# Performance work log

Hardware: AMD Instinct MI355X
Metric: run time of the kernel (lower is better)

The kernel has to match this reference:

```python
import jax, jax.numpy as jnp
import numpy as np

# The original module wraps a CvxpyLayer solving, per batch element:
#   min_y  c^T y - sum(entr(y) + entr(1-y))   (use_entropy=True)
#   s.t.   a' y + b' >= 0,  lb <= y <= ub
# where the wrapper passes a' = -a, b' = -b, i.e. the constraints are a y + b <= 0,
# with lb=0, ub=1. With binary entropy regularization the KKT stationarity gives
# the closed form y*(lam) = sigmoid(-(c + a^T lam)) for dual vars lam >= 0, and the
# dual is maximized by projected gradient ascent (grad = a y* + b). This is the
# standard smooth/batched-GPU-friendly formulation of the same convex program.

NUM_ITERS = 100  # fixed dual ascent iterations (jit-friendly)
STEP = 0.05      # dual step size


def _solve(a, b, c):
    # a: [B, M, N], b: [B, M], c: [B, N]
    def body(lam, _):
        # y*(lam) = sigmoid(-(c + a^T lam))   [B, N]
        y = jax.nn.sigmoid(-(c + jnp.einsum('bmn,bm->bn', a, lam)))
        # dual gradient: a y + b               [B, M]
        g = jnp.einsum('bmn,bn->bm', a, y) + b
        lam = jnp.maximum(lam + STEP * g, 0.0)
        return lam, None

    lam0 = jnp.zeros_like(b)
    lam, _ = jax.lax.scan(body, lam0, None, length=NUM_ITERS)
    y = jax.nn.sigmoid(-(c + jnp.einsum('bmn,bm->bn', a, lam)))
    return y


def setup_inputs() -> dict:
    key = jax.random.key(0)
    ka, kb, kc = jax.random.split(key, 3)
    B, M, N = 2048, 128, 256
    a = jax.random.normal(ka, (B, M, N), dtype=jnp.float32)
    b = jax.random.normal(kb, (B, M), dtype=jnp.float32)
    c = jax.random.normal(kc, (B, N), dtype=jnp.float32)
    return {"a": a, "b": b, "c": c}


def reference(a, b, c):
    y = _solve(a, b, c).astype(jnp.float32)
    status = jnp.zeros((a.shape[0],), dtype=jnp.int32)
    return (y, status)
```

## Files before the change

kernel.cpp:

```cpp
#include <hip/hip_runtime.h>


#define BB 2048
#define MM 128
#define NN 256

__global__ __launch_bounds__(512, 2) void cvx_dual_ascent(
    const float* __restrict__ A,
    const float* __restrict__ Bv,
    const float* __restrict__ C,
    float* __restrict__ out)
{
    const int bi  = blockIdx.x;
    const int tid = threadIdx.x;
    const int w   = tid >> 6;
    const int l   = tid & 63;
    const int c   = tid >> 1;
    const int myrow = (l >> 1) & 15;

    __shared__ float zp_s[8][260];
    __shared__ float y_s[NN];
    __shared__ float lam_s[8][16];
    __shared__ float scr_s[512];

    const float* Ab = A + (size_t)bi * (MM * NN);
    unsigned long long a0  = (unsigned long long)(Ab + (16*w + 0)  * NN + 4*l);
    unsigned long long a4  = (unsigned long long)(Ab + (16*w + 4)  * NN + 4*l);
    unsigned long long a8  = (unsigned long long)(Ab + (16*w + 8)  * NN + 4*l);
    unsigned long long a12 = (unsigned long long)(Ab + (16*w + 12) * NN + 4*l);
    unsigned lamrd = (unsigned)(size_t)&lam_s[w][0];
    unsigned zpw   = (unsigned)(size_t)&zp_s[w][4*l];
    unsigned zprd  = (unsigned)(size_t)&zp_s[(tid & 1) * 4][c];
    unsigned ysw   = (unsigned)(size_t)&y_s[c];
    unsigned ysr   = (unsigned)(size_t)&y_s[4*l];
    unsigned lamw  = (unsigned)(size_t)&lam_s[w][myrow];
    unsigned scw   = (unsigned)(size_t)&scr_s[tid];
    unsigned scrd  = (unsigned)(size_t)&scr_s[tid ^ 32];
    unsigned long long outa = (unsigned long long)(out + (size_t)bi * NN + c);
    float cr  = C[bi * NN + c];
    float sbv = 0.05f * Bv[bi * MM + 16*w + myrow];
    float lam = 0.f;
    int   cnt = 100;

    if (tid < 128) lam_s[tid >> 4][tid & 15] = 0.f;
    __syncthreads();

    asm volatile(
        "global_load_dwordx4 v[36:39], %[a0], off\n\t"
        "global_load_dwordx4 v[40:43], %[a0], off offset:1024\n\t"
        "global_load_dwordx4 v[44:47], %[a0], off offset:2048\n\t"
        "global_load_dwordx4 v[48:51], %[a0], off offset:3072\n\t"
        "global_load_dwordx4 v[52:55], %[a4], off\n\t"
        "global_load_dwordx4 v[56:59], %[a4], off offset:1024\n\t"
        "global_load_dwordx4 v[60:63], %[a4], off offset:2048\n\t"
        "global_load_dwordx4 v[64:67], %[a4], off offset:3072\n\t"
        "global_load_dwordx4 v[68:71], %[a8], off\n\t"
        "global_load_dwordx4 v[72:75], %[a8], off offset:1024\n\t"
        "global_load_dwordx4 v[76:79], %[a8], off offset:2048\n\t"
        "global_load_dwordx4 v[80:83], %[a8], off offset:3072\n\t"
        "global_load_dwordx4 v[84:87], %[a12], off\n\t"
        "global_load_dwordx4 v[88:91], %[a12], off offset:1024\n\t"
        "global_load_dwordx4 v[92:95], %[a12], off offset:2048\n\t"
        "global_load_dwordx4 v[96:99], %[a12], off offset:3072\n\t"
        "s_waitcnt vmcnt(0)\n\t"
        ".LTOP%=:\n\t"
        "ds_read_b128 v[100:103], %[lamrd]\n\t"
        "ds_read_b128 v[104:107], %[lamrd] offset:16\n\t"
        "ds_read_b128 v[108:111], %[lamrd] offset:32\n\t"
        "ds_read_b128 v[112:115], %[lamrd] offset:48\n\t"
        "s_waitcnt lgkmcnt(0)\n\t"
        "v_mul_f32 v116, v36, v100\n\t"
        "v_mul_f32 v117, v37, v100\n\t"
        "v_mul_f32 v118, v38, v100\n\t"
        "v_mul_f32 v119, v39, v100\n\t"
        "v_fmac_f32 v116, v40, v101\n\t"
        "v_fmac_f32 v117, v41, v101\n\t"
        "v_fmac_f32 v118, v42, v101\n\t"
        "v_fmac_f32 v119, v43, v101\n\t"
        "v_fmac_f32 v116, v44, v102\n\t"
        "v_fmac_f32 v117, v45, v102\n\t"
        "v_fmac_f32 v118, v46, v102\n\t"
        "v_fmac_f32 v119, v47, v102\n\t"
        "v_fmac_f32 v116, v48, v103\n\t"
        "v_fmac_f32 v117, v49, v103\n\t"
        "v_fmac_f32 v118, v50, v103\n\t"
        "v_fmac_f32 v119, v51, v103\n\t"
        "v_fmac_f32 v116, v52, v104\n\t"
        "v_fmac_f32 v117, v53, v104\n\t"
        "v_fmac_f32 v118, v54, v104\n\t"
        "v_fmac_f32 v119, v55, v104\n\t"
        "v_fmac_f32 v116, v56, v105\n\t"
        "v_fmac_f32 v117, v57, v105\n\t"
        "v_fmac_f32 v118, v58, v105\n\t"
        "v_fmac_f32 v119, v59, v105\n\t"
        "v_fmac_f32 v116, v60, v106\n\t"
        "v_fmac_f32 v117, v61, v106\n\t"
        "v_fmac_f32 v118, v62, v106\n\t"
        "v_fmac_f32 v119, v63, v106\n\t"
        "v_fmac_f32 v116, v64, v107\n\t"
        "v_fmac_f32 v117, v65, v107\n\t"
        "v_fmac_f32 v118, v66, v107\n\t"
        "v_fmac_f32 v119, v67, v107\n\t"
        "v_fmac_f32 v116, v68, v108\n\t"
        "v_fmac_f32 v117, v69, v108\n\t"
        "v_fmac_f32 v118, v70, v108\n\t"
        "v_fmac_f32 v119, v71, v108\n\t"
        "v_fmac_f32 v116, v72, v109\n\t"
        "v_fmac_f32 v117, v73, v109\n\t"
        "v_fmac_f32 v118, v74, v109\n\t"
        "v_fmac_f32 v119, v75, v109\n\t"
        "v_fmac_f32 v116, v76, v110\n\t"
        "v_fmac_f32 v117, v77, v110\n\t"
        "v_fmac_f32 v118, v78, v110\n\t"
        "v_fmac_f32 v119, v79, v110\n\t"
        "v_fmac_f32 v116, v80, v111\n\t"
        "v_fmac_f32 v117, v81, v111\n\t"
        "v_fmac_f32 v118, v82, v111\n\t"
        "v_fmac_f32 v119, v83, v111\n\t"
        "v_fmac_f32 v116, v84, v112\n\t"
        "v_fmac_f32 v117, v85, v112\n\t"
        "v_fmac_f32 v118, v86, v112\n\t"
        "v_fmac_f32 v119, v87, v112\n\t"
        "v_fmac_f32 v116, v88, v113\n\t"
        "v_fmac_f32 v117, v89, v113\n\t"
        "v_fmac_f32 v118, v90, v113\n\t"
        "v_fmac_f32 v119, v91, v113\n\t"
        "v_fmac_f32 v116, v92, v114\n\t"
        "v_fmac_f32 v117, v93, v114\n\t"
        "v_fmac_f32 v118, v94, v114\n\t"
        "v_fmac_f32 v119, v95, v114\n\t"
        "v_fmac_f32 v116, v96, v115\n\t"
        "v_fmac_f32 v117, v97, v115\n\t"
        "v_fmac_f32 v118, v98, v115\n\t"
        "v_fmac_f32 v119, v99, v115\n\t"
        "ds_write_b128 %[zpw], v[116:119]\n\t"
        "s_waitcnt lgkmcnt(0)\n\t"
        "s_barrier\n\t"
        "ds_read_b32 v120, %[zprd]\n\t"
        "ds_read_b32 v121, %[zprd] offset:1040\n\t"
        "ds_read_b32 v122, %[zprd] offset:2080\n\t"
        "ds_read_b32 v123, %[zprd] offset:3120\n\t"
        "s_waitcnt lgkmcnt(0)\n\t"
        "v_add_f32 v120, v120, v121\n\t"
        "v_add_f32 v122, v122, v123\n\t"
        "v_add_f32 v120, v120, v122\n\t"
        "ds_swizzle_b32 v121, v120 offset:0x041F\n\t"
        "s_waitcnt lgkmcnt(0)\n\t"
        "v_add_f32 v120, v120, v121\n\t"
        "v_add_f32 v121, %[cr], v120\n\t"
        "v_mul_f32 v121, %[l2e], v121\n\t"
        "v_exp_f32 v121, v121\n\t"
        "s_nop 1\n\t"
        "v_add_f32 v121, 1.0, v121\n\t"
        "v_rcp_f32 v121, v121\n\t"
        "s_nop 1\n\t"
        "s_cmp_eq_u32 %[cnt], 0\n\t"
        "s_cbranch_scc1 .LEXIT%=\n\t"
        "ds_write_b32 %[ysw], v121\n\t"
        "s_waitcnt lgkmcnt(0)\n\t"
        "s_barrier\n\t"
        "ds_read_b128 v[116:119], %[ysr]\n\t"
        "s_waitcnt lgkmcnt(0)\n\t"
        "v_mul_f32 v100, v36, v116\n\t"
        "v_mul_f32 v101, v40, v116\n\t"
        "v_mul_f32 v102, v44, v116\n\t"
        "v_mul_f32 v103, v48, v116\n\t"
        "v_mul_f32 v104, v52, v116\n\t"
        "v_mul_f32 v105, v56, v116\n\t"
        "v_mul_f32 v106, v60, v116\n\t"
        "v_mul_f32 v107, v64, v116\n\t"
        "v_mul_f32 v108, v68, v116\n\t"
        "v_mul_f32 v109, v72, v116\n\t"
        "v_mul_f32 v110, v76, v116\n\t"
        "v_mul_f32 v111, v80, v116\n\t"
        "v_mul_f32 v112, v84, v116\n\t"
        "v_mul_f32 v113, v88, v116\n\t"
        "v_mul_f32 v114, v92, v116\n\t"
        "v_mul_f32 v115, v96, v116\n\t"
        "v_fmac_f32 v100, v37, v117\n\t"
        "v_fmac_f32 v101, v41, v117\n\t"
        "v_fmac_f32 v102, v45, v117\n\t"
        "v_fmac_f32 v103, v49, v117\n\t"
        "v_fmac_f32 v104, v53, v117\n\t"
        "v_fmac_f32 v105, v57, v117\n\t"
        "v_fmac_f32 v106, v61, v117\n\t"
        "v_fmac_f32 v107, v65, v117\n\t"
        "v_fmac_f32 v108, v69, v117\n\t"
        "v_fmac_f32 v109, v73, v117\n\t"
        "v_fmac_f32 v110, v77, v117\n\t"
        "v_fmac_f32 v111, v81, v117\n\t"
        "v_fmac_f32 v112, v85, v117\n\t"
        "v_fmac_f32 v113, v89, v117\n\t"
        "v_fmac_f32 v114, v93, v117\n\t"
        "v_fmac_f32 v115, v97, v117\n\t"
        "v_fmac_f32 v100, v38, v118\n\t"
        "v_fmac_f32 v101, v42, v118\n\t"
        "v_fmac_f32 v102, v46, v118\n\t"
        "v_fmac_f32 v103, v50, v118\n\t"
        "v_fmac_f32 v104, v54, v118\n\t"
        "v_fmac_f32 v105, v58, v118\n\t"
        "v_fmac_f32 v106, v62, v118\n\t"
        "v_fmac_f32 v107, v66, v118\n\t"
        "v_fmac_f32 v108, v70, v118\n\t"
        "v_fmac_f32 v109, v74, v118\n\t"
        "v_fmac_f32 v110, v78, v118\n\t"
        "v_fmac_f32 v111, v82, v118\n\t"
        "v_fmac_f32 v112, v86, v118\n\t"
        "v_fmac_f32 v113, v90, v118\n\t"
        "v_fmac_f32 v114, v94, v118\n\t"
        "v_fmac_f32 v115, v98, v118\n\t"
        "v_fmac_f32 v100, v39, v119\n\t"
        "v_fmac_f32 v101, v43, v119\n\t"
        "v_fmac_f32 v102, v47, v119\n\t"
        "v_fmac_f32 v103, v51, v119\n\t"
        "v_fmac_f32 v104, v55, v119\n\t"
        "v_fmac_f32 v105, v59, v119\n\t"
        "v_fmac_f32 v106, v63, v119\n\t"
        "v_fmac_f32 v107, v67, v119\n\t"
        "v_fmac_f32 v108, v71, v119\n\t"
        "v_fmac_f32 v109, v75, v119\n\t"
        "v_fmac_f32 v110, v79, v119\n\t"
        "v_fmac_f32 v111, v83, v119\n\t"
        "v_fmac_f32 v112, v87, v119\n\t"
        "v_fmac_f32 v113, v91, v119\n\t"
        "v_fmac_f32 v114, v95, v119\n\t"
        "v_fmac_f32 v115, v99, v119\n\t"
        "v_cndmask_b32 v120, v100, v108, %[mb4]\n\t"
        "v_cndmask_b32 v121, v101, v109, %[mb4]\n\t"
        "v_cndmask_b32 v122, v102, v110, %[mb4]\n\t"
        "v_cndmask_b32 v123, v103, v111, %[mb4]\n\t"
        "v_cndmask_b32 v124, v108, v100, %[mb4]\n\t"
        "v_cndmask_b32 v125, v109, v101, %[mb4]\n\t"
        "v_cndmask_b32 v126, v110, v102, %[mb4]\n\t"
        "v_cndmask_b32 v127, v111, v103, %[mb4]\n\t"
        "ds_swizzle_b32 v124, v124 offset:0x401F\n\t"
        "ds_swizzle_b32 v125, v125 offset:0x401F\n\t"
        "ds_swizzle_b32 v126, v126 offset:0x401F\n\t"
        "ds_swizzle_b32 v127, v127 offset:0x401F\n\t"
        "v_cndmask_b32 v116, v104, v112, %[mb4]\n\t"
        "v_cndmask_b32 v117, v105, v113, %[mb4]\n\t"
        "v_cndmask_b32 v118, v106, v114, %[mb4]\n\t"
        "v_cndmask_b32 v119, v107, v115, %[mb4]\n\t"
        "v_cndmask_b32 v108, v112, v104, %[mb4]\n\t"
        "v_cndmask_b32 v109, v113, v105, %[mb4]\n\t"
        "v_cndmask_b32 v110, v114, v106, %[mb4]\n\t"
        "v_cndmask_b32 v111, v115, v107, %[mb4]\n\t"
        "ds_swizzle_b32 v108, v108 offset:0x401F\n\t"
        "ds_swizzle_b32 v109, v109 offset:0x401F\n\t"
        "ds_swizzle_b32 v110, v110 offset:0x401F\n\t"
        "ds_swizzle_b32 v111, v111 offset:0x401F\n\t"
        "s_waitcnt lgkmcnt(0)\n\t"
        "v_add_f32 v100, v120, v124\n\t"
        "v_add_f32 v101, v121, v125\n\t"
        "v_add_f32 v102, v122, v126\n\t"
        "v_add_f32 v103, v123, v127\n\t"
        "v_add_f32 v104, v116, v108\n\t"
        "v_add_f32 v105, v117, v109\n\t"
        "v_add_f32 v106, v118, v110\n\t"
        "v_add_f32 v107, v119, v111\n\t"
        "v_cndmask_b32 v120, v100, v104, %[mb3]\n\t"
        "v_cndmask_b32 v121, v101, v105, %[mb3]\n\t"
        "v_cndmask_b32 v122, v102, v106, %[mb3]\n\t"
        "v_cndmask_b32 v123, v103, v107, %[mb3]\n\t"
        "v_cndmask_b32 v124, v104, v100, %[mb3]\n\t"
        "v_cndmask_b32 v125, v105, v101, %[mb3]\n\t"
        "v_cndmask_b32 v126, v106, v102, %[mb3]\n\t"
        "v_cndmask_b32 v127, v107, v103, %[mb3]\n\t"
        "ds_swizzle_b32 v124, v124 offset:0x201F\n\t"
        "ds_swizzle_b32 v125, v125 offset:0x201F\n\t"
        "ds_swizzle_b32 v126, v126 offset:0x201F\n\t"
        "ds_swizzle_b32 v127, v127 offset:0x201F\n\t"
        "s_waitcnt lgkmcnt(0)\n\t"
        "v_add_f32 v100, v120, v124\n\t"
        "v_add_f32 v101, v121, v125\n\t"
        "v_add_f32 v102, v122, v126\n\t"
        "v_add_f32 v103, v123, v127\n\t"
        "v_cndmask_b32 v120, v100, v102, %[mb2]\n\t"
        "v_cndmask_b32 v121, v101, v103, %[mb2]\n\t"
        "v_cndmask_b32 v122, v102, v100, %[mb2]\n\t"
        "v_cndmask_b32 v123, v103, v101, %[mb2]\n\t"
        "ds_swizzle_b32 v122, v122 offset:0x101F\n\t"
        "ds_swizzle_b32 v123, v123 offset:0x101F\n\t"
        "s_waitcnt lgkmcnt(0)\n\t"
        "v_add_f32 v100, v120, v122\n\t"
        "v_add_f32 v101, v121, v123\n\t"
        "v_cndmask_b32 v120, v100, v101, %[mb1]\n\t"
        "v_cndmask_b32 v121, v101, v100, %[mb1]\n\t"
        "ds_swizzle_b32 v121, v121 offset:0x081F\n\t"
        "s_waitcnt lgkmcnt(0)\n\t"
        "v_add_f32 v100, v120, v121\n\t"
        "ds_swizzle_b32 v101, v100 offset:0x041F\n\t"
        "s_waitcnt lgkmcnt(0)\n\t"
        "v_add_f32 v100, v100, v101\n\t"
        "ds_write_b32 %[scw], v100\n\t"
        "s_waitcnt lgkmcnt(0)\n\t"
        "ds_read_b32 v101, %[scrd]\n\t"
        "s_waitcnt lgkmcnt(0)\n\t"
        "v_add_f32 v100, v100, v101\n\t"
        "v_fmac_f32 %[lam], %[step], v100\n\t"
        "v_add_f32 %[lam], %[sb], %[lam]\n\t"
        "v_max_f32 %[lam], 0, %[lam]\n\t"
        "ds_write_b32 %[lamw], %[lam]\n\t"
        "s_waitcnt lgkmcnt(0)\n\t"
        "s_sub_u32 %[cnt], %[cnt], 1\n\t"
        "s_branch .LTOP%=\n\t"
        ".LEXIT%=:\n\t"
        "global_store_dword %[outa], v121, off\n\t"
        "s_waitcnt vmcnt(0)\n\t"
        : [lam] "+v"(lam), [cnt] "+s"(cnt)
        : [a0] "v"(a0), [a4] "v"(a4), [a8] "v"(a8), [a12] "v"(a12),
          [lamrd] "v"(lamrd), [zpw] "v"(zpw), [zprd] "v"(zprd),
          [ysw] "v"(ysw), [ysr] "v"(ysr), [lamw] "v"(lamw),
          [scw] "v"(scw), [scrd] "v"(scrd), [outa] "v"(outa),
          [cr] "v"(cr), [sb] "v"(sbv),
          [step] "s"(0.05f), [l2e] "s"(1.4426950408889634f),
          [mb4] "s"(0xFFFF0000FFFF0000ull), [mb3] "s"(0xFF00FF00FF00FF00ull),
          [mb2] "s"(0xF0F0F0F0F0F0F0F0ull), [mb1] "s"(0xCCCCCCCCCCCCCCCCull)
        : "memory", "scc",
          "v36","v37","v38","v39","v40","v41","v42","v43","v44","v45",
          "v46","v47","v48","v49","v50","v51","v52","v53","v54","v55",
          "v56","v57","v58","v59","v60","v61","v62","v63","v64","v65",
          "v66","v67","v68","v69","v70","v71","v72","v73","v74","v75",
          "v76","v77","v78","v79","v80","v81","v82","v83","v84","v85",
          "v86","v87","v88","v89","v90","v91","v92","v93","v94","v95",
          "v96","v97","v98","v99","v100","v101","v102","v103","v104",
          "v105","v106","v107","v108","v109","v110","v111","v112","v113",
          "v114","v115","v116","v117","v118","v119","v120","v121","v122",
          "v123","v124","v125","v126","v127");

    if (tid == 0) out[(size_t)BB * NN + bi] = 0.0f;
}

extern "C" void kernel_launch(void* const* d_in, const int* in_sizes, int n_in,
                              void* d_out, int out_size, void* d_ws, size_t ws_size,
                              hipStream_t stream) {
    const float* A  = (const float*)d_in[0];
    const float* Bv = (const float*)d_in[1];
    const float* C  = (const float*)d_in[2];
    float* out = (float*)d_out;

    cvx_dual_ascent<<<dim3(BB), dim3(512), 0, stream>>>(A, Bv, C, out);
}
```

Measured before the change: 511.0 us.

## Keep dual variables in SGPRs and replace LDS swizzle reductions with DPP/permlane

The per-iteration lambda broadcast through LDS (ds_write, ds_read_b128 ×4) is replaced by v_readlane into 16 SGPRs, which are then used directly as scalar operands in the A^T·lam FMAs. The butterfly reduction for the A·y gradient is rebuilt around v_permlane32_swap and v_permlane16_swap, with DPP row_ror and quad_perm replacing most ds_swizzle ops and the LDS scratch exchange. The lane-to-row mapping changes so each row's result lands in lanes spaced four apart. This removes LDS round-trips and lgkmcnt waits from the serial 100-iteration loop, at the cost of readlane latency, extra s_nop hazard padding and 16 clobbered SGPRs.

```diff
diff --git a/kernel.cpp b/kernel.cpp
--- a/kernel.cpp
+++ b/kernel.cpp
@@ -16,33 +16,26 @@
     const int w   = tid >> 6;
     const int l   = tid & 63;
     const int c   = tid >> 1;
-    const int myrow = (l >> 1) & 15;
+    const int myrow = (l >> 2) & 15;
 
     __shared__ float zp_s[8][260];
     __shared__ float y_s[NN];
-    __shared__ float lam_s[8][16];
-    __shared__ float scr_s[512];
 
     const float* Ab = A + (size_t)bi * (MM * NN);
     unsigned long long a0  = (unsigned long long)(Ab + (16*w + 0)  * NN + 4*l);
     unsigned long long a4  = (unsigned long long)(Ab + (16*w + 4)  * NN + 4*l);
     unsigned long long a8  = (unsigned long long)(Ab + (16*w + 8)  * NN + 4*l);
     unsigned long long a12 = (unsigned long long)(Ab + (16*w + 12) * NN + 4*l);
-    unsigned lamrd = (unsigned)(size_t)&lam_s[w][0];
     unsigned zpw   = (unsigned)(size_t)&zp_s[w][4*l];
     unsigned zprd  = (unsigned)(size_t)&zp_s[(tid & 1) * 4][c];
     unsigned ysw   = (unsigned)(size_t)&y_s[c];
     unsigned ysr   = (unsigned)(size_t)&y_s[4*l];
-    unsigned lamw  = (unsigned)(size_t)&lam_s[w][myrow];
-    unsigned scw   = (unsigned)(size_t)&scr_s[tid];
-    unsigned scrd  = (unsigned)(size_t)&scr_s[tid ^ 32];
     unsigned long long outa = (unsigned long long)(out + (size_t)bi * NN + c);
     float cr  = C[bi * NN + c];
     float sbv = 0.05f * Bv[bi * MM + 16*w + myrow];
     float lam = 0.f;
     int   cnt = 100;
 
-    if (tid < 128) lam_s[tid >> 4][tid & 15] = 0.f;
     __syncthreads();
 
     asm volatile(
@@ -62,77 +55,80 @@
         "global_load_dwordx4 v[88:91], %[a12], off offset:1024\n\t"
         "global_load_dwordx4 v[92:95], %[a12], off offset:2048\n\t"
         "global_load_dwordx4 v[96:99], %[a12], off offset:3072\n\t"
+        "s_mov_b32 s80, 0\n\t"  "s_mov_b32 s81, 0\n\t"
+        "s_mov_b32 s82, 0\n\t"  "s_mov_b32 s83, 0\n\t"
+        "s_mov_b32 s84, 0\n\t"  "s_mov_b32 s85, 0\n\t"
+        "s_mov_b32 s86, 0\n\t"  "s_mov_b32 s87, 0\n\t"
+        "s_mov_b32 s88, 0\n\t"  "s_mov_b32 s89, 0\n\t"
+        "s_mov_b32 s90, 0\n\t"  "s_mov_b32 s91, 0\n\t"
+        "s_mov_b32 s92, 0\n\t"  "s_mov_b32 s93, 0\n\t"
+        "s_mov_b32 s94, 0\n\t"  "s_mov_b32 s95, 0\n\t"
         "s_waitcnt vmcnt(0)\n\t"
         ".LTOP%=:\n\t"
-        "ds_read_b128 v[100:103], %[lamrd]\n\t"
-        "ds_read_b128 v[104:107], %[lamrd] offset:16\n\t"
-        "ds_read_b128 v[108:111], %[lamrd] offset:32\n\t"
-        "ds_read_b128 v[112:115], %[lamrd] offset:48\n\t"
-        "s_waitcnt lgkmcnt(0)\n\t"
-        "v_mul_f32 v116, v36, v100\n\t"
-        "v_mul_f32 v117, v37, v100\n\t"
-        "v_mul_f32 v118, v38, v100\n\t"
-        "v_mul_f32 v119, v39, v100\n\t"
-        "v_fmac_f32 v116, v40, v101\n\t"
-        "v_fmac_f32 v117, v41, v101\n\t"
-        "v_fmac_f32 v118, v42, v101\n\t"
-        "v_fmac_f32 v119, v43, v101\n\t"
-        "v_fmac_f32 v116, v44, v102\n\t"
-        "v_fmac_f32 v117, v45, v102\n\t"
-        "v_fmac_f32 v118, v46, v102\n\t"
-        "v_fmac_f32 v119, v47, v102\n\t"
-        "v_fmac_f32 v116, v48, v103\n\t"
-        "v_fmac_f32 v117, v49, v103\n\t"
-        "v_fmac_f32 v118, v50, v103\n\t"
-        "v_fmac_f32 v119, v51, v103\n\t"
-        "v_fmac_f32 v116, v52, v104\n\t"
-        "v_fmac_f32 v117, v53, v104\n\t"
-        "v_fmac_f32 v118, v54, v104\n\t"
-        "v_fmac_f32 v119, v55, v104\n\t"
-        "v_fmac_f32 v116, v56, v105\n\t"
-        "v_fmac_f32 v117, v57, v105\n\t"
-        "v_fmac_f32 v118, v58, v105\n\t"
-        "v_fmac_f32 v119, v59, v105\n\t"
-        "v_fmac_f32 v116, v60, v106\n\t"
-        "v_fmac_f32 v117, v61, v106\n\t"
-        "v_fmac_f32 v118, v62, v106\n\t"
-        "v_fmac_f32 v119, v63, v106\n\t"
-        "v_fmac_f32 v116, v64, v107\n\t"
-        "v_fmac_f32 v117, v65, v107\n\t"
-        "v_fmac_f32 v118, v66, v107\n\t"
-        "v_fmac_f32 v119, v67, v107\n\t"
-        "v_fmac_f32 v116, v68, v108\n\t"
-        "v_fmac_f32 v117, v69, v108\n\t"
-        "v_fmac_f32 v118, v70, v108\n\t"
-        "v_fmac_f32 v119, v71, v108\n\t"
-        "v_fmac_f32 v116, v72, v109\n\t"
-        "v_fmac_f32 v117, v73, v109\n\t"
-        "v_fmac_f32 v118, v74, v109\n\t"
-        "v_fmac_f32 v119, v75, v109\n\t"
-        "v_fmac_f32 v116, v76, v110\n\t"
-        "v_fmac_f32 v117, v77, v110\n\t"
-        "v_fmac_f32 v118, v78, v110\n\t"
-        "v_fmac_f32 v119, v79, v110\n\t"
-        "v_fmac_f32 v116, v80, v111\n\t"
-        "v_fmac_f32 v117, v81, v111\n\t"
-        "v_fmac_f32 v118, v82, v111\n\t"
-        "v_fmac_f32 v119, v83, v111\n\t"
-        "v_fmac_f32 v116, v84, v112\n\t"
-        "v_fmac_f32 v117, v85, v112\n\t"
-        "v_fmac_f32 v118, v86, v112\n\t"
-        "v_fmac_f32 v119, v87, v112\n\t"
-        "v_fmac_f32 v116, v88, v113\n\t"
-        "v_fmac_f32 v117, v89, v113\n\t"
-        "v_fmac_f32 v118, v90, v113\n\t"
-        "v_fmac_f32 v119, v91, v113\n\t"
-        "v_fmac_f32 v116, v92, v114\n\t"
-        "v_fmac_f32 v117, v93, v114\n\t"
-        "v_fmac_f32 v118, v94, v114\n\t"
-        "v_fmac_f32 v119, v95, v114\n\t"
-        "v_fmac_f32 v116, v96, v115\n\t"
-        "v_fmac_f32 v117, v97, v115\n\t"
-        "v_fmac_f32 v118, v98, v115\n\t"
-        "v_fmac_f32 v119, v99, v115\n\t"
+        "v_mul_f32 v116, s80, v36\n\t"
+        "v_mul_f32 v117, s80, v37\n\t"
+        "v_mul_f32 v118, s80, v38\n\t"
+        "v_mul_f32 v119, s80, v39\n\t"
+        "v_fmac_f32 v116, s81, v40\n\t"
+        "v_fmac_f32 v117, s81, v41\n\t"
+        "v_fmac_f32 v118, s81, v42\n\t"
+        "v_fmac_f32 v119, s81, v43\n\t"
+        "v_fmac_f32 v116, s82, v44\n\t"
+        "v_fmac_f32 v117, s82, v45\n\t"
+        "v_fmac_f32 v118, s82, v46\n\t"
+        "v_fmac_f32 v119, s82, v47\n\t"
+        "v_fmac_f32 v116, s83, v48\n\t"
+        "v_fmac_f32 v117, s83, v49\n\t"
+        "v_fmac_f32 v118, s83, v50\n\t"
+        "v_fmac_f32 v119, s83, v51\n\t"
+        "v_fmac_f32 v116, s84, v52\n\t"
+        "v_fmac_f32 v117, s84, v53\n\t"
+        "v_fmac_f32 v118, s84, v54\n\t"
+        "v_fmac_f32 v119, s84, v55\n\t"
+        "v_fmac_f32 v116, s85, v56\n\t"
+        "v_fmac_f32 v117, s85, v57\n\t"
+        "v_fmac_f32 v118, s85, v58\n\t"
+        "v_fmac_f32 v119, s85, v59\n\t"
+        "v_fmac_f32 v116, s86, v60\n\t"
+        "v_fmac_f32 v117, s86, v61\n\t"
+        "v_fmac_f32 v118, s86, v62\n\t"
+        "v_fmac_f32 v119, s86, v63\n\t"
+        "v_fmac_f32 v116, s87, v64\n\t"
+        "v_fmac_f32 v117, s87, v65\n\t"
+        "v_fmac_f32 v118, s87, v66\n\t"
+        "v_fmac_f32 v119, s87, v67\n\t"
+        "v_fmac_f32 v116, s88, v68\n\t"
+        "v_fmac_f32 v117, s88, v69\n\t"
+        "v_fmac_f32 v118, s88, v70\n\t"
+        "v_fmac_f32 v119, s88, v71\n\t"
+        "v_fmac_f32 v116, s89, v72\n\t"
+        "v_fmac_f32 v117, s89, v73\n\t"
+        "v_fmac_f32 v118, s89, v74\n\t"
+        "v_fmac_f32 v119, s89, v75\n\t"
+        "v_fmac_f32 v116, s90, v76\n\t"
+        "v_fmac_f32 v117, s90, v77\n\t"
+        "v_fmac_f32 v118, s90, v78\n\t"
+        "v_fmac_f32 v119, s90, v79\n\t"
+        "v_fmac_f32 v116, s91, v80\n\t"
+        "v_fmac_f32 v117, s91, v81\n\t"
+        "v_fmac_f32 v118, s91, v82\n\t"
+        "v_fmac_f32 v119, s91, v83\n\t"
+        "v_fmac_f32 v116, s92, v84\n\t"
+        "v_fmac_f32 v117, s92, v85\n\t"
+        "v_fmac_f32 v118, s92, v86\n\t"
+        "v_fmac_f32 v119, s92, v87\n\t"
+        "v_fmac_f32 v116, s93, v88\n\t"
+        "v_fmac_f32 v117, s93, v89\n\t"
+        "v_fmac_f32 v118, s93, v90\n\t"
+        "v_fmac_f32 v119, s93, v91\n\t"
+        "v_fmac_f32 v116, s94, v92\n\t"
+        "v_fmac_f32 v117, s94, v93\n\t"
+        "v_fmac_f32 v118, s94, v94\n\t"
+        "v_fmac_f32 v119, s94, v95\n\t"
+        "v_fmac_f32 v116, s95, v96\n\t"
+        "v_fmac_f32 v117, s95, v97\n\t"
+        "v_fmac_f32 v118, s95, v98\n\t"
+        "v_fmac_f32 v119, s95, v99\n\t"
         "ds_write_b128 %[zpw], v[116:119]\n\t"
         "s_waitcnt lgkmcnt(0)\n\t"
         "s_barrier\n\t"
@@ -144,8 +140,8 @@
         "v_add_f32 v120, v120, v121\n\t"
         "v_add_f32 v122, v122, v123\n\t"
         "v_add_f32 v120, v120, v122\n\t"
-        "ds_swizzle_b32 v121, v120 offset:0x041F\n\t"
-        "s_waitcnt lgkmcnt(0)\n\t"
+        "s_nop 1\n\t"
+        "v_mov_b32_dpp v121, v120 quad_perm:[1,0,3,2] row_mask:0xf bank_mask:0xf\n\t"
         "v_add_f32 v120, v120, v121\n\t"
         "v_add_f32 v121, %[cr], v120\n\t"
         "v_mul_f32 v121, %[l2e], v121\n\t"
@@ -225,83 +221,71 @@
         "v_fmac_f32 v113, v91, v119\n\t"
         "v_fmac_f32 v114, v95, v119\n\t"
         "v_fmac_f32 v115, v99, v119\n\t"
-        "v_cndmask_b32 v120, v100, v108, %[mb4]\n\t"
-        "v_cndmask_b32 v121, v101, v109, %[mb4]\n\t"
-        "v_cndmask_b32 v122, v102, v110, %[mb4]\n\t"
-        "v_cndmask_b32 v123, v103, v111, %[mb4]\n\t"
-        "v_cndmask_b32 v124, v108, v100, %[mb4]\n\t"
-        "v_cndmask_b32 v125, v109, v101, %[mb4]\n\t"
-        "v_cndmask_b32 v126, v110, v102, %[mb4]\n\t"
-        "v_cndmask_b32 v127, v111, v103, %[mb4]\n\t"
-        "ds_swizzle_b32 v124, v124 offset:0x401F\n\t"
-        "ds_swizzle_b32 v125, v125 offset:0x401F\n\t"
-        "ds_swizzle_b32 v126, v126 offset:0x401F\n\t"
-        "ds_swizzle_b32 v127, v127 offset:0x401F\n\t"
-        "v_cndmask_b32 v116, v104, v112, %[mb4]\n\t"
-        "v_cndmask_b32 v117, v105, v113, %[mb4]\n\t"
-        "v_cndmask_b32 v118, v106, v114, %[mb4]\n\t"
-        "v_cndmask_b32 v119, v107, v115, %[mb4]\n\t"
-        "v_cndmask_b32 v108, v112, v104, %[mb4]\n\t"
-        "v_cndmask_b32 v109, v113, v105, %[mb4]\n\t"
-        "v_cndmask_b32 v110, v114, v106, %[mb4]\n\t"
-        "v_cndmask_b32 v111, v115, v107, %[mb4]\n\t"
-        "ds_swizzle_b32 v108, v108 offset:0x401F\n\t"
-        "ds_swizzle_b32 v109, v109 offset:0x401F\n\t"
-        "ds_swizzle_b32 v110, v110 offset:0x401F\n\t"
-        "ds_swizzle_b32 v111, v111 offset:0x401F\n\t"
-        "s_waitcnt lgkmcnt(0)\n\t"
+        "s_nop 1\n\t"
+        "v_permlane32_swap_b32 v100, v108\n\t"
+        "v_permlane32_swap_b32 v101, v109\n\t"
+        "v_permlane32_swap_b32 v102, v110\n\t"
+        "v_permlane32_swap_b32 v103, v111\n\t"
+        "v_permlane32_swap_b32 v104, v112\n\t"
+        "v_permlane32_swap_b32 v105, v113\n\t"
+        "v_permlane32_swap_b32 v106, v114\n\t"
+        "v_permlane32_swap_b32 v107, v115\n\t"
+        "v_add_f32 v100, v100, v108\n\t"
+        "v_add_f32 v101, v101, v109\n\t"
+        "v_add_f32 v102, v102, v110\n\t"
+        "v_add_f32 v103, v103, v111\n\t"
+        "v_add_f32 v104, v104, v112\n\t"
+        "v_add_f32 v105, v105, v113\n\t"
+        "v_add_f32 v106, v106, v114\n\t"
+        "v_add_f32 v107, v107, v115\n\t"
+        "v_permlane16_swap_b32 v100, v104\n\t"
+        "v_permlane16_swap_b32 v101, v105\n\t"
+        "v_permlane16_swap_b32 v102, v106\n\t"
+        "v_permlane16_swap_b32 v103, v107\n\t"
+        "v_add_f32 v100, v100, v104\n\t"
+        "v_add_f32 v101, v101, v105\n\t"
+        "v_add_f32 v102, v102, v106\n\t"
+        "v_add_f32 v103, v103, v107\n\t"
+        "v_cndmask_b32 v120, v100, v102, %[mb3]\n\t"
+        "v_cndmask_b32 v121, v102, v100, %[mb3]\n\t"
+        "v_cndmask_b32 v122, v101, v103, %[mb3]\n\t"
+        "v_cndmask_b32 v123, v103, v101, %[mb3]\n\t"
+        "s_nop 1\n\t"
+        "v_mov_b32_dpp v124, v121 row_ror:8 row_mask:0xf bank_mask:0xf\n\t"
+        "v_mov_b32_dpp v125, v123 row_ror:8 row_mask:0xf bank_mask:0xf\n\t"
         "v_add_f32 v100, v120, v124\n\t"
-        "v_add_f32 v101, v121, v125\n\t"
-        "v_add_f32 v102, v122, v126\n\t"
-        "v_add_f32 v103, v123, v127\n\t"
-        "v_add_f32 v104, v116, v108\n\t"
-        "v_add_f32 v105, v117, v109\n\t"
-        "v_add_f32 v106, v118, v110\n\t"
-        "v_add_f32 v107, v119, v111\n\t"
-        "v_cndmask_b32 v120, v100, v104, %[mb3]\n\t"
-        "v_cndmask_b32 v121, v101, v105, %[mb3]\n\t"
-        "v_cndmask_b32 v122, v102, v106, %[mb3]\n\t"
-        "v_cndmask_b32 v123, v103, v107, %[mb3]\n\t"
-        "v_cndmask_b32 v124, v104, v100, %[mb3]\n\t"
-        "v_cndmask_b32 v125, v105, v101, %[mb3]\n\t"
-        "v_cndmask_b32 v126, v106, v102, %[mb3]\n\t"
-        "v_cndmask_b32 v127, v107, v103, %[mb3]\n\t"
-        "ds_swizzle_b32 v124, v124 offset:0x201F\n\t"
-        "ds_swizzle_b32 v125, v125 offset:0x201F\n\t"
-        "ds_swizzle_b32 v126, v126 offset:0x201F\n\t"
-        "ds_swizzle_b32 v127, v127 offset:0x201F\n\t"
-        "s_waitcnt lgkmcnt(0)\n\t"
-        "v_add_f32 v100, v120, v124\n\t"
-        "v_add_f32 v101, v121, v125\n\t"
-        "v_add_f32 v102, v122, v126\n\t"
-        "v_add_f32 v103, v123, v127\n\t"
-        "v_cndmask_b32 v120, v100, v102, %[mb2]\n\t"
-        "v_cndmask_b32 v121, v101, v103, %[mb2]\n\t"
-        "v_cndmask_b32 v122, v102, v100, %[mb2]\n\t"
-        "v_cndmask_b32 v123, v103, v101, %[mb2]\n\t"
-        "ds_swizzle_b32 v122, v122 offset:0x101F\n\t"
-        "ds_swizzle_b32 v123, v123 offset:0x101F\n\t"
-        "s_waitcnt lgkmcnt(0)\n\t"
-        "v_add_f32 v100, v120, v122\n\t"
-        "v_add_f32 v101, v121, v123\n\t"
-        "v_cndmask_b32 v120, v100, v101, %[mb1]\n\t"
-        "v_cndmask_b32 v121, v101, v100, %[mb1]\n\t"
-        "ds_swizzle_b32 v121, v121 offset:0x081F\n\t"
+        "v_add_f32 v101, v122, v125\n\t"
+        "v_cndmask_b32 v120, v100, v101, %[mb2]\n\t"
+        "v_cndmask_b32 v121, v101, v100, %[mb2]\n\t"
+        "ds_swizzle_b32 v121, v121 offset:0x101F\n\t"
         "s_waitcnt lgkmcnt(0)\n\t"
         "v_add_f32 v100, v120, v121\n\t"
-        "ds_swizzle_b32 v101, v100 offset:0x041F\n\t"
-        "s_waitcnt lgkmcnt(0)\n\t"
-        "v_add_f32 v100, v100, v101\n\t"
-        "ds_write_b32 %[scw], v100\n\t"
-        "s_waitcnt lgkmcnt(0)\n\t"
-        "ds_read_b32 v101, %[scrd]\n\t"
-        "s_waitcnt lgkmcnt(0)\n\t"
-        "v_add_f32 v100, v100, v101\n\t"
+        "s_nop 1\n\t"
+        "v_mov_b32_dpp v121, v100 quad_perm:[2,3,0,1] row_mask:0xf bank_mask:0xf\n\t"
+        "v_add_f32 v100, v100, v121\n\t"
+        "s_nop 1\n\t"
+        "v_mov_b32_dpp v121, v100 quad_perm:[1,0,3,2] row_mask:0xf bank_mask:0xf\n\t"
+        "v_add_f32 v100, v100, v121\n\t"
         "v_fmac_f32 %[lam], %[step], v100\n\t"
         "v_add_f32 %[lam], %[sb], %[lam]\n\t"
         "v_max_f32 %[lam], 0, %[lam]\n\t"
-        "ds_write_b32 %[lamw], %[lam]\n\t"
-        "s_waitcnt lgkmcnt(0)\n\t"
+        "s_nop 1\n\t"
+        "v_readlane_b32 s80, %[lam], 0\n\t"
+        "v_readlane_b32 s81, %[lam], 4\n\t"
+        "v_readlane_b32 s82, %[lam], 8\n\t"
+        "v_readlane_b32 s83, %[lam], 12\n\t"
+        "v_readlane_b32 s84, %[lam], 16\n\t"
+        "v_readlane_b32 s85, %[lam], 20\n\t"
+        "v_readlane_b32 s86, %[lam], 24\n\t"
+        "v_readlane_b32 s87, %[lam], 28\n\t"
+        "v_readlane_b32 s88, %[lam], 32\n\t"
+        "v_readlane_b32 s89, %[lam], 36\n\t"
+        "v_readlane_b32 s90, %[lam], 40\n\t"
+        "v_readlane_b32 s91, %[lam], 44\n\t"
+        "v_readlane_b32 s92, %[lam], 48\n\t"
+        "v_readlane_b32 s93, %[lam], 52\n\t"
+        "v_readlane_b32 s94, %[lam], 56\n\t"
+        "v_readlane_b32 s95, %[lam], 60\n\t"
         "s_sub_u32 %[cnt], %[cnt], 1\n\t"
         "s_branch .LTOP%=\n\t"
         ".LEXIT%=:\n\t"
@@ -309,14 +293,14 @@
         "s_waitcnt vmcnt(0)\n\t"
         : [lam] "+v"(lam), [cnt] "+s"(cnt)
         : [a0] "v"(a0), [a4] "v"(a4), [a8] "v"(a8), [a12] "v"(a12),
-          [lamrd] "v"(lamrd), [zpw] "v"(zpw), [zprd] "v"(zprd),
-          [ysw] "v"(ysw), [ysr] "v"(ysr), [lamw] "v"(lamw),
-          [scw] "v"(scw), [scrd] "v"(scrd), [outa] "v"(outa),
+          [zpw] "v"(zpw), [zprd] "v"(zprd),
+          [ysw] "v"(ysw), [ysr] "v"(ysr), [outa] "v"(outa),
           [cr] "v"(cr), [sb] "v"(sbv),
           [step] "s"(0.05f), [l2e] "s"(1.4426950408889634f),
-          [mb4] "s"(0xFFFF0000FFFF0000ull), [mb3] "s"(0xFF00FF00FF00FF00ull),
-          [mb2] "s"(0xF0F0F0F0F0F0F0F0ull), [mb1] "s"(0xCCCCCCCCCCCCCCCCull)
+          [mb3] "s"(0xFF00FF00FF00FF00ull), [mb2] "s"(0xF0F0F0F0F0F0F0F0ull)
         : "memory", "scc",
+          "s80","s81","s82","s83","s84","s85","s86","s87",
+          "s88","s89","s90","s91","s92","s93","s94","s95",
           "v36","v37","v38","v39","v40","v41","v42","v43","v44","v45",
           "v46","v47","v48","v49","v50","v51","v52","v53","v54","v55",
           "v56","v57","v58","v59","v60","v61","v62","v63","v64","v65",
```

Measured after the change: 539.7 us. 1.06x slower.

## Compute sigmoid redundantly per wave to drop second barrier; double-buffer partials; permlane reductions

Applied to the files above, without the earlier changes.

Each wave now reads all eight waves' partial z-sums directly (double-buffered shared array toggled by xor) and computes the full 256-element sigmoid vector locally, eliminating the y_s write/barrier/read round trip per iteration. The cross-lane row reduction is rebuilt using permlane32/permlane16 swaps and DPP moves instead of chains of ds_swizzle and LDS scratch exchange. This trades one barrier and several LDS round trips per iteration for redundant exp/rcp work across waves and more LDS read bandwidth; only wave 0 stores the output.

```diff
diff --git a/kernel.cpp b/kernel.cpp
--- a/kernel.cpp
+++ b/kernel.cpp
@@ -15,13 +15,10 @@
     const int tid = threadIdx.x;
     const int w   = tid >> 6;
     const int l   = tid & 63;
-    const int c   = tid >> 1;
-    const int myrow = (l >> 1) & 15;
-
-    __shared__ float zp_s[8][260];
-    __shared__ float y_s[NN];
+    const int myrow = (l >> 2) & 15;
+
+    __shared__ float zp2_s[2][8][256];
     __shared__ float lam_s[8][16];
-    __shared__ float scr_s[512];
 
     const float* Ab = A + (size_t)bi * (MM * NN);
     unsigned long long a0  = (unsigned long long)(Ab + (16*w + 0)  * NN + 4*l);
@@ -29,23 +26,24 @@
     unsigned long long a8  = (unsigned long long)(Ab + (16*w + 8)  * NN + 4*l);
     unsigned long long a12 = (unsigned long long)(Ab + (16*w + 12) * NN + 4*l);
     unsigned lamrd = (unsigned)(size_t)&lam_s[w][0];
-    unsigned zpw   = (unsigned)(size_t)&zp_s[w][4*l];
-    unsigned zprd  = (unsigned)(size_t)&zp_s[(tid & 1) * 4][c];
-    unsigned ysw   = (unsigned)(size_t)&y_s[c];
-    unsigned ysr   = (unsigned)(size_t)&y_s[4*l];
+    unsigned zpw   = (unsigned)(size_t)&zp2_s[0][w][4*l];
+    unsigned zprd  = (unsigned)(size_t)&zp2_s[0][0][4*l];
     unsigned lamw  = (unsigned)(size_t)&lam_s[w][myrow];
-    unsigned scw   = (unsigned)(size_t)&scr_s[tid];
-    unsigned scrd  = (unsigned)(size_t)&scr_s[tid ^ 32];
-    unsigned long long outa = (unsigned long long)(out + (size_t)bi * NN + c);
-    float cr  = C[bi * NN + c];
+    unsigned long long outa = (unsigned long long)(out + (size_t)bi * NN + 4*l);
+    const float4 c4 = *reinterpret_cast<const float4*>(&C[bi * NN + 4*l]);
+    float c0 = c4.x, c1 = c4.y, c2 = c4.z, c3 = c4.w;
     float sbv = 0.05f * Bv[bi * MM + 16*w + myrow];
     float lam = 0.f;
+    float wvf = (float)0;
+    int   wvv = w;
     int   cnt = 100;
+    (void)wvf;
 
     if (tid < 128) lam_s[tid >> 4][tid & 15] = 0.f;
     __syncthreads();
 
     asm volatile(
+        "v_readfirstlane_b32 s78, %[wvv]\n\t"
         "global_load_dwordx4 v[36:39], %[a0], off\n\t"
         "global_load_dwordx4 v[40:43], %[a0], off offset:1024\n\t"
         "global_load_dwordx4 v[44:47], %[a0], off offset:2048\n\t"
@@ -136,31 +134,70 @@
         "ds_write_b128 %[zpw], v[116:119]\n\t"
         "s_waitcnt lgkmcnt(0)\n\t"
         "s_barrier\n\t"
-        "ds_read_b32 v120, %[zprd]\n\t"
-        "ds_read_b32 v121, %[zprd] offset:1040\n\t"
-        "ds_read_b32 v122, %[zprd] offset:2080\n\t"
-        "ds_read_b32 v123, %[zprd] offset:3120\n\t"
-        "s_waitcnt lgkmcnt(0)\n\t"
-        "v_add_f32 v120, v120, v121\n\t"
-        "v_add_f32 v122, v122, v123\n\t"
-        "v_add_f32 v120, v120, v122\n\t"
-        "ds_swizzle_b32 v121, v120 offset:0x041F\n\t"
-        "s_waitcnt lgkmcnt(0)\n\t"
-        "v_add_f32 v120, v120, v121\n\t"
-        "v_add_f32 v121, %[cr], v120\n\t"
-        "v_mul_f32 v121, %[l2e], v121\n\t"
-        "v_exp_f32 v121, v121\n\t"
-        "s_nop 1\n\t"
-        "v_add_f32 v121, 1.0, v121\n\t"
-        "v_rcp_f32 v121, v121\n\t"
+        "ds_read_b128 v[100:103], %[zprd]\n\t"
+        "ds_read_b128 v[104:107], %[zprd] offset:1024\n\t"
+        "ds_read_b128 v[108:111], %[zprd] offset:2048\n\t"
+        "ds_read_b128 v[112:115], %[zprd] offset:3072\n\t"
+        "ds_read_b128 v[120:123], %[zprd] offset:4096\n\t"
+        "ds_read_b128 v[124:127], %[zprd] offset:5120\n\t"
+        "s_waitcnt lgkmcnt(0)\n\t"
+        "v_add_f32 v100, v100, v104\n\t"
+        "v_add_f32 v101, v101, v105\n\t"
+        "v_add_f32 v102, v102, v106\n\t"
+        "v_add_f32 v103, v103, v107\n\t"
+        "v_add_f32 v108, v108, v112\n\t"
+        "v_add_f32 v109, v109, v113\n\t"
+        "v_add_f32 v110, v110, v114\n\t"
+        "v_add_f32 v111, v111, v115\n\t"
+        "v_add_f32 v120, v120, v124\n\t"
+        "v_add_f32 v121, v121, v125\n\t"
+        "v_add_f32 v122, v122, v126\n\t"
+        "v_add_f32 v123, v123, v127\n\t"
+        "v_add_f32 v100, v100, v108\n\t"
+        "v_add_f32 v101, v101, v109\n\t"
+        "v_add_f32 v102, v102, v110\n\t"
+        "v_add_f32 v103, v103, v111\n\t"
+        "ds_read_b128 v[104:107], %[zprd] offset:6144\n\t"
+        "ds_read_b128 v[108:111], %[zprd] offset:7168\n\t"
+        "v_add_f32 v100, v100, v120\n\t"
+        "v_add_f32 v101, v101, v121\n\t"
+        "v_add_f32 v102, v102, v122\n\t"
+        "v_add_f32 v103, v103, v123\n\t"
+        "s_waitcnt lgkmcnt(0)\n\t"
+        "v_add_f32 v104, v104, v108\n\t"
+        "v_add_f32 v105, v105, v109\n\t"
+        "v_add_f32 v106, v106, v110\n\t"
+        "v_add_f32 v107, v107, v111\n\t"
+        "v_add_f32 v100, v100, v104\n\t"
+        "v_add_f32 v101, v101, v105\n\t"
+        "v_add_f32 v102, v102, v106\n\t"
+        "v_add_f32 v103, v103, v107\n\t"
+        "v_xor_b32 %[zpw], 0x2000, %[zpw]\n\t"
+        "v_xor_b32 %[zprd], 0x2000, %[zprd]\n\t"
+        "v_add_f32 v116, %[c0], v100\n\t"
+        "v_add_f32 v117, %[c1], v101\n\t"
+        "v_add_f32 v118, %[c2], v102\n\t"
+        "v_add_f32 v119, %[c3], v103\n\t"
+        "v_mul_f32 v116, %[l2e], v116\n\t"
+        "v_mul_f32 v117, %[l2e], v117\n\t"
+        "v_mul_f32 v118, %[l2e], v118\n\t"
+        "v_mul_f32 v119, %[l2e], v119\n\t"
+        "v_exp_f32 v116, v116\n\t"
+        "v_exp_f32 v117, v117\n\t"
+        "v_exp_f32 v118, v118\n\t"
+        "v_exp_f32 v119, v119\n\t"
+        "s_nop 1\n\t"
+        "v_add_f32 v116, 1.0, v116\n\t"
+        "v_add_f32 v117, 1.0, v117\n\t"
+        "v_add_f32 v118, 1.0, v118\n\t"
+        "v_add_f32 v119, 1.0, v119\n\t"
+        "v_rcp_f32 v116, v116\n\t"
+        "v_rcp_f32 v117, v117\n\t"
+        "v_rcp_f32 v118, v118\n\t"
+        "v_rcp_f32 v119, v119\n\t"
         "s_nop 1\n\t"
         "s_cmp_eq_u32 %[cnt], 0\n\t"
         "s_cbranch_scc1 .LEXIT%=\n\t"
-        "ds_write_b32 %[ysw], v121\n\t"
-        "s_waitcnt lgkmcnt(0)\n\t"
-        "s_barrier\n\t"
-        "ds_read_b128 v[116:119], %[ysr]\n\t"
-        "s_waitcnt lgkmcnt(0)\n\t"
         "v_mul_f32 v100, v36, v116\n\t"
         "v_mul_f32 v101, v40, v116\n\t"
         "v_mul_f32 v102, v44, v116\n\t"
@@ -225,98 +262,71 @@
         "v_fmac_f32 v113, v91, v119\n\t"
         "v_fmac_f32 v114, v95, v119\n\t"
         "v_fmac_f32 v115, v99, v119\n\t"
-        "v_cndmask_b32 v120, v100, v108, %[mb4]\n\t"
-        "v_cndmask_b32 v121, v101, v109, %[mb4]\n\t"
-        "v_cndmask_b32 v122, v102, v110, %[mb4]\n\t"
-        "v_cndmask_b32 v123, v103, v111, %[mb4]\n\t"
-        "v_cndmask_b32 v124, v108, v100, %[mb4]\n\t"
-        "v_cndmask_b32 v125, v109, v101, %[mb4]\n\t"
-        "v_cndmask_b32 v126, v110, v102, %[mb4]\n\t"
-        "v_cndmask_b32 v127, v111, v103, %[mb4]\n\t"
-        "ds_swizzle_b32 v124, v124 offset:0x401F\n\t"
-        "ds_swizzle_b32 v125, v125 offset:0x401F\n\t"
-        "ds_swizzle_b32 v126, v126 offset:0x401F\n\t"
-        "ds_swizzle_b32 v127, v127 offset:0x401F\n\t"
-        "v_cndmask_b32 v116, v104, v112, %[mb4]\n\t"
-        "v_cndmask_b32 v117, v105, v113, %[mb4]\n\t"
-        "v_cndmask_b32 v118, v106, v114, %[mb4]\n\t"
-        "v_cndmask_b32 v119, v107, v115, %[mb4]\n\t"
-        "v_cndmask_b32 v108, v112, v104, %[mb4]\n\t"
-        "v_cndmask_b32 v109, v113, v105, %[mb4]\n\t"
-        "v_cndmask_b32 v110, v114, v106, %[mb4]\n\t"
-        "v_cndmask_b32 v111, v115, v107, %[mb4]\n\t"
-        "ds_swizzle_b32 v108, v108 offset:0x401F\n\t"
-        "ds_swizzle_b32 v109, v109 offset:0x401F\n\t"
-        "ds_swizzle_b32 v110, v110 offset:0x401F\n\t"
-        "ds_swizzle_b32 v111, v111 offset:0x401F\n\t"
-        "s_waitcnt lgkmcnt(0)\n\t"
+        "s_nop 1\n\t"
+        "v_permlane32_swap_b32 v100, v108\n\t"
+        "v_permlane32_swap_b32 v101, v109\n\t"
+        "v_permlane32_swap_b32 v102, v110\n\t"
+        "v_permlane32_swap_b32 v103, v111\n\t"
+        "v_permlane32_swap_b32 v104, v112\n\t"
+        "v_permlane32_swap_b32 v105, v113\n\t"
+        "v_permlane32_swap_b32 v106, v114\n\t"
+        "v_permlane32_swap_b32 v107, v115\n\t"
+        "v_add_f32 v100, v100, v108\n\t"
+        "v_add_f32 v101, v101, v109\n\t"
+        "v_add_f32 v102, v102, v110\n\t"
+        "v_add_f32 v103, v103, v111\n\t"
+        "v_add_f32 v104, v104, v112\n\t"
+        "v_add_f32 v105, v105, v113\n\t"
+        "v_add_f32 v106, v106, v114\n\t"
+        "v_add_f32 v107, v107, v115\n\t"
+        "v_permlane16_swap_b32 v100, v104\n\t"
+        "v_permlane16_swap_b32 v101, v105\n\t"
+        "v_permlane16_swap_b32 v102, v106\n\t"
+        "v_permlane16_swap_b32 v103, v107\n\t"
+        "v_add_f32 v100, v100, v104\n\t"
+        "v_add_f32 v101, v101, v105\n\t"
+        "v_add_f32 v102, v102, v106\n\t"
+        "v_add_f32 v103, v103, v107\n\t"
+        "v_cndmask_b32 v120, v100, v102, %[mb3]\n\t"
+        "v_cndmask_b32 v121, v102, v100, %[mb3]\n\t"
+        "v_cndmask_b32 v122, v101, v103, %[mb3]\n\t"
+        "v_cndmask_b32 v123, v103, v101, %[mb3]\n\t"
+        "s_nop 1\n\t"
+        "v_mov_b32_dpp v124, v121 row_ror:8 row_mask:0xf bank_mask:0xf\n\t"
+        "v_mov_b32_dpp v125, v123 row_ror:8 row_mask:0xf bank_mask:0xf\n\t"
         "v_add_f32 v100, v120, v124\n\t"
-        "v_add_f32 v101, v121, v125\n\t"
-        "v_add_f32 v102, v122, v126\n\t"
-        "v_add_f32 v103, v123, v127\n\t"
-        "v_add_f32 v104, v116, v108\n\t"
-        "v_add_f32 v105, v117, v109\n\t"
-        "v_add_f32 v106, v118, v110\n\t"
-        "v_add_f32 v107, v119, v111\n\t"
-        "v_cndmask_b32 v120, v100, v104, %[mb3]\n\t"
-        "v_cndmask_b32 v121, v101, v105, %[mb3]\n\t"
-        "v_cndmask_b32 v122, v102, v106, %[mb3]\n\t"
-        "v_cndmask_b32 v123, v103, v107, %[mb3]\n\t"
-        "v_cndmask_b32 v124, v104, v100, %[mb3]\n\t"
-        "v_cndmask_b32 v125, v105, v101, %[mb3]\n\t"
-        "v_cndmask_b32 v126, v106, v102, %[mb3]\n\t"
-        "v_cndmask_b32 v127, v107, v103, %[mb3]\n\t"
-        "ds_swizzle_b32 v124, v124 offset:0x201F\n\t"
-        "ds_swizzle_b32 v125, v125 offset:0x201F\n\t"
-        "ds_swizzle_b32 v126, v126 offset:0x201F\n\t"
-        "ds_swizzle_b32 v127, v127 offset:0x201F\n\t"
-        "s_waitcnt lgkmcnt(0)\n\t"
-        "v_add_f32 v100, v120, v124\n\t"
-        "v_add_f32 v101, v121, v125\n\t"
-        "v_add_f32 v102, v122, v126\n\t"
-        "v_add_f32 v103, v123, v127\n\t"
-        "v_cndmask_b32 v120, v100, v102, %[mb2]\n\t"
-        "v_cndmask_b32 v121, v101, v103, %[mb2]\n\t"
-        "v_cndmask_b32 v122, v102, v100, %[mb2]\n\t"
-        "v_cndmask_b32 v123, v103, v101, %[mb2]\n\t"
-        "ds_swizzle_b32 v122, v122 offset:0x101F\n\t"
-        "ds_swizzle_b32 v123, v123 offset:0x101F\n\t"
-        "s_waitcnt lgkmcnt(0)\n\t"
-        "v_add_f32 v100, v120, v122\n\t"
-        "v_add_f32 v101, v121, v123\n\t"
-        "v_cndmask_b32 v120, v100, v101, %[mb1]\n\t"
-        "v_cndmask_b32 v121, v101, v100, %[mb1]\n\t"
-        "ds_swizzle_b32 v121, v121 offset:0x081F\n\t"
+        "v_add_f32 v101, v122, v125\n\t"
+        "v_cndmask_b32 v120, v100, v101, %[mb2]\n\t"
+        "v_cndmask_b32 v121, v101, v100, %[mb2]\n\t"
+        "ds_swizzle_b32 v121, v121 offset:0x101F\n\t"
         "s_waitcnt lgkmcnt(0)\n\t"
         "v_add_f32 v100, v120, v121\n\t"
-        "ds_swizzle_b32 v101, v100 offset:0x041F\n\t"
-        "s_waitcnt lgkmcnt(0)\n\t"
-        "v_add_f32 v100, v100, v101\n\t"
-        "ds_write_b32 %[scw], v100\n\t"
-        "s_waitcnt lgkmcnt(0)\n\t"
-        "ds_read_b32 v101, %[scrd]\n\t"
-        "s_waitcnt lgkmcnt(0)\n\t"
-        "v_add_f32 v100, v100, v101\n\t"
+        "s_nop 1\n\t"
+        "v_mov_b32_dpp v121, v100 quad_perm:[2,3,0,1] row_mask:0xf bank_mask:0xf\n\t"
+        "v_add_f32 v100, v100, v121\n\t"
+        "s_nop 1\n\t"
+        "v_mov_b32_dpp v121, v100 quad_perm:[1,0,3,2] row_mask:0xf bank_mask:0xf\n\t"
+        "v_add_f32 v100, v100, v121\n\t"
         "v_fmac_f32 %[lam], %[step], v100\n\t"
         "v_add_f32 %[lam], %[sb], %[lam]\n\t"
         "v_max_f32 %[lam], 0, %[lam]\n\t"
         "ds_write_b32 %[lamw], %[lam]\n\t"
-        "s_waitcnt lgkmcnt(0)\n\t"
         "s_sub_u32 %[cnt], %[cnt], 1\n\t"
         "s_branch .LTOP%=\n\t"
         ".LEXIT%=:\n\t"
-        "global_store_dword %[outa], v121, off\n\t"
+        "s_cmp_lg_u32 s78, 0\n\t"
+        "s_cbranch_scc1 .LSKIP%=\n\t"
+        "global_store_dwordx4 %[outa], v[116:119], off\n\t"
+        ".LSKIP%=:\n\t"
         "s_waitcnt vmcnt(0)\n\t"
-        : [lam] "+v"(lam), [cnt] "+s"(cnt)
+        : [lam] "+v"(lam), [cnt] "+s"(cnt), [zpw] "+v"(zpw), [zprd] "+v"(zprd)
         : [a0] "v"(a0), [a4] "v"(a4), [a8] "v"(a8), [a12] "v"(a12),
-          [lamrd] "v"(lamrd), [zpw] "v"(zpw), [zprd] "v"(zprd),
-          [ysw] "v"(ysw), [ysr] "v"(ysr), [lamw] "v"(lamw),
-          [scw] "v"(scw), [scrd] "v"(scrd), [outa] "v"(outa),
-          [cr] "v"(cr), [sb] "v"(sbv),
+          [lamrd] "v"(lamrd), [lamw] "v"(lamw), [outa] "v"(outa),
+          [c0] "v"(c0), [c1] "v"(c1), [c2] "v"(c2), [c3] "v"(c3),
+          [sb] "v"(sbv), [wvv] "v"(wvv),
           [step] "s"(0.05f), [l2e] "s"(1.4426950408889634f),
-          [mb4] "s"(0xFFFF0000FFFF0000ull), [mb3] "s"(0xFF00FF00FF00FF00ull),
-          [mb2] "s"(0xF0F0F0F0F0F0F0F0ull), [mb1] "s"(0xCCCCCCCCCCCCCCCCull)
-        : "memory", "scc",
+          [mb3] "s"(0xFF00FF00FF00FF00ull), [mb2] "s"(0xF0F0F0F0F0F0F0F0ull)
+        : "memory", "scc", "s78",
           "v36","v37","v38","v39","v40","v41","v42","v43","v44","v45",
           "v46","v47","v48","v49","v50","v51","v52","v53","v54","v55",
           "v56","v57","v58","v59","v60","v61","v62","v63","v64","v65",
```

Result: slower. 600.5 us (+17.5%).
